# Optimization experiments

Hardware: AMD Instinct MI355X
Metric: run time of the kernel (lower is better)

## Reference

```python
import jax, jax.numpy as jnp
import numpy as np

# LSNNParameters defaults (norse)
TAU_SYN_INV = 200.0     # 1/tau_syn
TAU_MEM_INV = 100.0     # 1/tau_mem
TAU_ADAPT_INV = 1.0 / 800.0  # 1/tau_adapt
V_LEAK = 0.0
V_TH = 1.0
V_RESET = 0.0
BETA = 1.8
DT = 0.001

B, IN_F, OUT_F = 8192, 512, 1024


def setup_inputs() -> dict:
    key = jax.random.key(0)
    k0, k1, k2, k3, k4, k5, k6 = jax.random.split(key, 7)
    input_spikes = (jax.random.uniform(k0, (B, IN_F)) < 0.2).astype(jnp.float32)
    z = (jax.random.uniform(k1, (B, OUT_F)) < 0.2).astype(jnp.float32)
    v = jax.random.normal(k2, (B, OUT_F)) * 0.5
    i = jax.random.normal(k3, (B, OUT_F)) * 0.5
    b = jax.random.uniform(k4, (B, OUT_F))
    input_weights = jax.random.normal(k5, (OUT_F, IN_F)) / np.sqrt(IN_F)
    recurrent_weights = jax.random.normal(k6, (OUT_F, OUT_F))
    return {
        "input_spikes": input_spikes,
        "z": z,
        "v": v,
        "i": i,
        "b": b,
        "input_weights": input_weights,
        "recurrent_weights": recurrent_weights,
    }


def reference(input_spikes, z, v, i, b, input_weights, recurrent_weights):
    # One euler step of the LSNN cell (norse lsnn_step).
    # voltage update: dv = dt * tau_mem_inv * ((v_leak - v) + i)
    v_decayed = v + DT * TAU_MEM_INV * ((V_LEAK - v) + i)
    # current decay: di = -dt * tau_syn_inv * i
    i_decayed = i + DT * (-TAU_SYN_INV) * i
    # adaptive threshold relaxes toward v_th
    b_decayed = b + DT * TAU_ADAPT_INV * (V_TH - b)
    # spike condition (heaviside jump)
    z_new = (v_decayed - b_decayed > 0).astype(v.dtype)
    # reset
    v_new = (1.0 - z_new) * v_decayed + z_new * V_RESET
    # current jumps from input + recurrent synapses (x @ W^T, torch linear)
    i_new = (
        i_decayed
        + jnp.einsum("bi,oi->bo", input_spikes, input_weights)
        + jnp.einsum("bo,no->bn", z, recurrent_weights)
    )
    # threshold adaptation
    b_new = b_decayed + z_new * TAU_ADAPT_INV * BETA
    # stack (z, v, i, b) new state -> [4, B, OUT_F]
    return jnp.stack([z_new, v_new, i_new, b_new])
```

## Files before the change

kernel.cpp:

```cpp
#include <hip/hip_runtime.h>

#define B_ROWS 8192
#define IN_F 512
#define OUT_F 1024
#define K_TOT 1536

#define BM 64
#define BN 64
#define BK 64
#define NITER (K_TOT / BK)

#define A4_COUNT (B_ROWS * (K_TOT / 4))
#define W4_COUNT (OUT_F  * (K_TOT / 4))
#define CAST_BLOCKS ((A4_COUNT + W4_COUNT) / 1024)
#define GEMM_BLOCKS ((B_ROWS / BM) * (OUT_F / BN))

typedef short bfrag __attribute__((ext_vector_type(8)));
typedef float f4    __attribute__((ext_vector_type(4)));

__device__ __forceinline__ unsigned int pack2bf(float a, float b) {
    unsigned int ua = __float_as_uint(a);
    unsigned int ub = __float_as_uint(b);
    ua = (ua + 0x7fffu + ((ua >> 16) & 1u)) >> 16;
    ub = (ub + 0x7fffu + ((ub >> 16) & 1u)) & 0xffff0000u;
    return ua | ub;
}

__global__ __launch_bounds__(256) void precast_aw(
    const float* __restrict__ spikes, const float* __restrict__ zin,
    const float* __restrict__ Wi,     const float* __restrict__ Wr,
    unsigned short* __restrict__ Abf, unsigned short* __restrict__ Wbf)
{
    const int base = blockIdx.x * 1024 + threadIdx.x;
    const float4* src[4];
    #pragma unroll
    for (int k = 0; k < 4; ++k) {
        const int idx = base + k * 256;
        if (idx < A4_COUNT) {
            const int row = idx / 384, c4 = idx - row * 384;
            src[k] = (const float4*)((c4 < 128)
                         ? spikes + (size_t)row * IN_F + c4 * 4
                         : zin    + (size_t)row * OUT_F + (c4 - 128) * 4);
        } else {
            const int w = idx - A4_COUNT;
            const int row = w / 384, c4 = w - row * 384;
            src[k] = (const float4*)((c4 < 128)
                         ? Wi + (size_t)row * IN_F + c4 * 4
                         : Wr + (size_t)row * OUT_F + (c4 - 128) * 4);
        }
    }
    float4 val[4];
    #pragma unroll
    for (int k = 0; k < 4; ++k) val[k] = *src[k];
    #pragma unroll
    for (int k = 0; k < 4; ++k) {
        const int idx = base + k * 256;
        unsigned short* dst = (idx < A4_COUNT)
                                  ? Abf + (size_t)idx * 4
                                  : Wbf + (size_t)(idx - A4_COUNT) * 4;
        uint2 pk = { pack2bf(val[k].x, val[k].y), pack2bf(val[k].z, val[k].w) };
        *(uint2*)dst = pk;
    }
}

__global__ __launch_bounds__(256, 4) void lsnn_gemm(
    const unsigned short* __restrict__ Abf,
    const unsigned short* __restrict__ Wbf,
    const float* __restrict__ vin,
    const float* __restrict__ iin,
    const float* __restrict__ bin,
    float* __restrict__ out)
{
    __shared__ unsigned short As[2][BM * BK];
    __shared__ unsigned short Ws[2][BN * BK];

    const int tid = threadIdx.x;
    const int bid = blockIdx.x;

    const int pw = bid * 1024 + tid;
    const f4* v4 = (const f4*)vin;
    const f4* i4 = (const f4*)iin;
    const f4* b4 = (const f4*)bin;
    f4 vv[4], ii[4], bb[4];
    #pragma unroll
    for (int k = 0; k < 4; ++k) vv[k] = v4[pw + k * 256];
    #pragma unroll
    for (int k = 0; k < 4; ++k) ii[k] = i4[pw + k * 256];
    #pragma unroll
    for (int k = 0; k < 4; ++k) bb[k] = b4[pw + k * 256];

    const int n0 = (bid & 15) * BN;
    const int m0 = (bid >> 4) * BM;

    const int lane = tid & 63;
    const int wave = tid >> 6;
    const int wm = (wave >> 1) * 32;
    const int wn = (wave & 1) * 32;
    const int lr = lane & 15;
    const int lq = lane >> 4;

    f4 acc[2][2];
    #pragma unroll
    for (int a = 0; a < 2; ++a)
        #pragma unroll
        for (int b = 0; b < 2; ++b)
            acc[a][b] = (f4)0.0f;

    const unsigned short* Ab = Abf + (size_t)m0 * K_TOT;
    const unsigned short* Wb = Wbf + (size_t)n0 * K_TOT;

    int rr[2], cc_[2], jj[2];
    #pragma unroll
    for (int p = 0; p < 2; ++p) {
        const int q = p * 256 + wave * 64 + lane;
        rr[p] = q >> 3;
        cc_[p] = (q & 7) ^ (rr[p] & 7);
        jj[p] = p * 256 + wave * 64;
    }

    auto stage = [&](int buf, int kt) {
        #pragma unroll
        for (int p = 0; p < 2; ++p)
            __builtin_amdgcn_global_load_lds(
                (const __attribute__((address_space(1))) void*)(Ab + (size_t)rr[p] * K_TOT + kt + cc_[p] * 8),
                (__attribute__((address_space(3))) void*)(&As[buf][jj[p] * 8]),
                16, 0, 0);
        #pragma unroll
        for (int p = 0; p < 2; ++p)
            __builtin_amdgcn_global_load_lds(
                (const __attribute__((address_space(1))) void*)(Wb + (size_t)rr[p] * K_TOT + kt + cc_[p] * 8),
                (__attribute__((address_space(3))) void*)(&Ws[buf][jj[p] * 8]),
                16, 0, 0);
    };

    stage(0, 0);
    __syncthreads();

    int cur = 0;
    for (int it = 0; it < NITER; ++it) {
        if (it + 1 < NITER) stage(cur ^ 1, (it + 1) * BK);

        #pragma unroll
        for (int ks = 0; ks < 2; ++ks) {
            const int cc = ks * 4 + lq;
            bfrag af[2], wf[2];
            #pragma unroll
            for (int t = 0; t < 2; ++t) {
                const int row = wm + t * 16 + lr;
                af[t] = *(const bfrag*)&As[cur][row * BK + ((cc ^ (row & 7)) << 3)];
            }
            #pragma unroll
            for (int t = 0; t < 2; ++t) {
                const int row = wn + t * 16 + lr;
                wf[t] = *(const bfrag*)&Ws[cur][row * BK + ((cc ^ (row & 7)) << 3)];
            }
            #pragma unroll
            for (int tm = 0; tm < 2; ++tm)
                #pragma unroll
                for (int tn = 0; tn < 2; ++tn)
                    acc[tm][tn] = __builtin_amdgcn_mfma_f32_16x16x32_bf16(
                        af[tm], wf[tn], acc[tm][tn], 0, 0, 0);
        }

        __syncthreads();
        cur ^= 1;
    }

    const size_t PL = (size_t)B_ROWS * OUT_F;
    #pragma unroll
    for (int k = 0; k < 4; ++k) {
        f4 z, vn, bn;
        #pragma unroll
        for (int c = 0; c < 4; ++c) {
            const float v_dec = vv[k][c] + 0.1f * (ii[k][c] - vv[k][c]);
            const float b_dec = bb[k][c] + 1.25e-06f * (1.0f - bb[k][c]);
            const float zz = (v_dec - b_dec > 0.0f) ? 1.0f : 0.0f;
            z[c]  = zz;
            vn[c] = (1.0f - zz) * v_dec;
            bn[c] = b_dec + zz * 0.00225f;
        }
        const int j = pw + k * 256;
        __builtin_nontemporal_store(z,  (f4*)out + j);
        __builtin_nontemporal_store(vn, (f4*)(out + PL) + j);
        __builtin_nontemporal_store(bn, (f4*)(out + 3 * PL) + j);
    }

    const size_t PL2 = 2 * PL;
    #pragma unroll
    for (int tm = 0; tm < 2; ++tm) {
        #pragma unroll
        for (int tn = 0; tn < 2; ++tn) {
            #pragma unroll
            for (int r = 0; r < 4; ++r) {
                const int gm = m0 + wm + tm * 16 + lq * 4 + r;
                const int gn = n0 + wn + tn * 16 + lr;
                const size_t idx = (size_t)gm * OUT_F + gn;
                const float i = iin[idx];
                __builtin_nontemporal_store((i - 0.2f * i) + acc[tm][tn][r],
                                            &out[PL2 + idx]);
            }
        }
    }
}

extern "C" void kernel_launch(void* const* d_in, const int* in_sizes, int n_in,
                              void* d_out, int out_size, void* d_ws, size_t ws_size,
                              hipStream_t stream) {
    const float* spikes = (const float*)d_in[0];
    const float* z      = (const float*)d_in[1];
    const float* v      = (const float*)d_in[2];
    const float* i      = (const float*)d_in[3];
    const float* b      = (const float*)d_in[4];
    const float* Wi     = (const float*)d_in[5];
    const float* Wr     = (const float*)d_in[6];
    float* out = (float*)d_out;

    unsigned short* Abf = (unsigned short*)d_ws;
    unsigned short* Wbf = Abf + (size_t)B_ROWS * K_TOT;

    precast_aw<<<CAST_BLOCKS, 256, 0, stream>>>(spikes, z, Wi, Wr, Abf, Wbf);

    lsnn_gemm<<<GEMM_BLOCKS, 256, 0, stream>>>(Abf, Wbf, v, i, b, out);
}
```

Before: 297.2 us.

## Halve GEMM K-tile, raise occupancy, and map elementwise state to the block's output tile

Reduces the K tile from 64 to 32, cutting LDS per block in half. It raises the launch-bounds occupancy hint from 4 to 8 blocks per CU and rewrites the LDS swizzle and staging to one 16-byte load per thread per operand. The elementwise v/i/b loads and z/v/b stores now cover the block's own 64x64 output tile instead of a contiguous flat chunk, which gives better locality with the i read in the epilogue. The cost is twice as many barrier-separated K iterations and less work per sync, and the higher occupancy target tightens the register budget.

```diff
diff --git a/kernel.cpp b/kernel.cpp
--- a/kernel.cpp
+++ b/kernel.cpp
@@ -7,7 +7,7 @@
 
 #define BM 64
 #define BN 64
-#define BK 64
+#define BK 32
 #define NITER (K_TOT / BK)
 
 #define A4_COUNT (B_ROWS * (K_TOT / 4))
@@ -63,7 +63,7 @@
     }
 }
 
-__global__ __launch_bounds__(256, 4) void lsnn_gemm(
+__global__ __launch_bounds__(256, 8) void lsnn_gemm(
     const unsigned short* __restrict__ Abf,
     const unsigned short* __restrict__ Wbf,
     const float* __restrict__ vin,
@@ -76,21 +76,25 @@
 
     const int tid = threadIdx.x;
     const int bid = blockIdx.x;
-
-    const int pw = bid * 1024 + tid;
+    const int n0 = (bid & 15) * BN;
+    const int m0 = (bid >> 4) * BM;
+
     const f4* v4 = (const f4*)vin;
     const f4* i4 = (const f4*)iin;
     const f4* b4 = (const f4*)bin;
+    size_t pidx[4];
+    #pragma unroll
+    for (int k = 0; k < 4; ++k) {
+        const int j = k * 256 + tid;
+        pidx[k] = (size_t)(m0 + (j >> 4)) * (OUT_F / 4) + (n0 >> 2) + (j & 15);
+    }
     f4 vv[4], ii[4], bb[4];
     #pragma unroll
-    for (int k = 0; k < 4; ++k) vv[k] = v4[pw + k * 256];
-    #pragma unroll
-    for (int k = 0; k < 4; ++k) ii[k] = i4[pw + k * 256];
-    #pragma unroll
-    for (int k = 0; k < 4; ++k) bb[k] = b4[pw + k * 256];
-
-    const int n0 = (bid & 15) * BN;
-    const int m0 = (bid >> 4) * BM;
+    for (int k = 0; k < 4; ++k) vv[k] = v4[pidx[k]];
+    #pragma unroll
+    for (int k = 0; k < 4; ++k) ii[k] = i4[pidx[k]];
+    #pragma unroll
+    for (int k = 0; k < 4; ++k) bb[k] = b4[pidx[k]];
 
     const int lane = tid & 63;
     const int wave = tid >> 6;
@@ -109,28 +113,20 @@
     const unsigned short* Ab = Abf + (size_t)m0 * K_TOT;
     const unsigned short* Wb = Wbf + (size_t)n0 * K_TOT;
 
-    int rr[2], cc_[2], jj[2];
-    #pragma unroll
-    for (int p = 0; p < 2; ++p) {
-        const int q = p * 256 + wave * 64 + lane;
-        rr[p] = q >> 3;
-        cc_[p] = (q & 7) ^ (rr[p] & 7);
-        jj[p] = p * 256 + wave * 64;
-    }
+    const int rS = tid >> 2;
+    const int cS = (tid & 3) ^ ((rS >> 1) & 3);
+    const unsigned short* Asrc = Ab + (size_t)rS * K_TOT + cS * 8;
+    const unsigned short* Wsrc = Wb + (size_t)rS * K_TOT + cS * 8;
 
     auto stage = [&](int buf, int kt) {
-        #pragma unroll
-        for (int p = 0; p < 2; ++p)
-            __builtin_amdgcn_global_load_lds(
-                (const __attribute__((address_space(1))) void*)(Ab + (size_t)rr[p] * K_TOT + kt + cc_[p] * 8),
-                (__attribute__((address_space(3))) void*)(&As[buf][jj[p] * 8]),
-                16, 0, 0);
-        #pragma unroll
-        for (int p = 0; p < 2; ++p)
-            __builtin_amdgcn_global_load_lds(
-                (const __attribute__((address_space(1))) void*)(Wb + (size_t)rr[p] * K_TOT + kt + cc_[p] * 8),
-                (__attribute__((address_space(3))) void*)(&Ws[buf][jj[p] * 8]),
-                16, 0, 0);
+        __builtin_amdgcn_global_load_lds(
+            (const __attribute__((address_space(1))) void*)(Asrc + kt),
+            (__attribute__((address_space(3))) void*)(&As[buf][tid * 8]),
+            16, 0, 0);
+        __builtin_amdgcn_global_load_lds(
+            (const __attribute__((address_space(1))) void*)(Wsrc + kt),
+            (__attribute__((address_space(3))) void*)(&Ws[buf][tid * 8]),
+            16, 0, 0);
     };
 
     stage(0, 0);
@@ -140,27 +136,23 @@
     for (int it = 0; it < NITER; ++it) {
         if (it + 1 < NITER) stage(cur ^ 1, (it + 1) * BK);
 
-        #pragma unroll
-        for (int ks = 0; ks < 2; ++ks) {
-            const int cc = ks * 4 + lq;
-            bfrag af[2], wf[2];
+        bfrag af[2], wf[2];
+        #pragma unroll
+        for (int t = 0; t < 2; ++t) {
+            const int row = wm + t * 16 + lr;
+            af[t] = *(const bfrag*)&As[cur][row * BK + ((lq ^ ((row >> 1) & 3)) << 3)];
+        }
+        #pragma unroll
+        for (int t = 0; t < 2; ++t) {
+            const int row = wn + t * 16 + lr;
+            wf[t] = *(const bfrag*)&Ws[cur][row * BK + ((lq ^ ((row >> 1) & 3)) << 3)];
+        }
+        #pragma unroll
+        for (int tm = 0; tm < 2; ++tm)
             #pragma unroll
-            for (int t = 0; t < 2; ++t) {
-                const int row = wm + t * 16 + lr;
-                af[t] = *(const bfrag*)&As[cur][row * BK + ((cc ^ (row & 7)) << 3)];
-            }
-            #pragma unroll
-            for (int t = 0; t < 2; ++t) {
-                const int row = wn + t * 16 + lr;
-                wf[t] = *(const bfrag*)&Ws[cur][row * BK + ((cc ^ (row & 7)) << 3)];
-            }
-            #pragma unroll
-            for (int tm = 0; tm < 2; ++tm)
-                #pragma unroll
-                for (int tn = 0; tn < 2; ++tn)
-                    acc[tm][tn] = __builtin_amdgcn_mfma_f32_16x16x32_bf16(
-                        af[tm], wf[tn], acc[tm][tn], 0, 0, 0);
-        }
+            for (int tn = 0; tn < 2; ++tn)
+                acc[tm][tn] = __builtin_amdgcn_mfma_f32_16x16x32_bf16(
+                    af[tm], wf[tn], acc[tm][tn], 0, 0, 0);
 
         __syncthreads();
         cur ^= 1;
@@ -179,10 +171,9 @@
             vn[c] = (1.0f - zz) * v_dec;
             bn[c] = b_dec + zz * 0.00225f;
         }
-        const int j = pw + k * 256;
-        __builtin_nontemporal_store(z,  (f4*)out + j);
-        __builtin_nontemporal_store(vn, (f4*)(out + PL) + j);
-        __builtin_nontemporal_store(bn, (f4*)(out + 3 * PL) + j);
+        __builtin_nontemporal_store(z,  (f4*)out + pidx[k]);
+        __builtin_nontemporal_store(vn, (f4*)(out + PL) + pidx[k]);
+        __builtin_nontemporal_store(bn, (f4*)(out + 3 * PL) + pidx[k]);
     }
 
     const size_t PL2 = 2 * PL;
```

Result: slower. 349.3 us (+17.5%).
